# Optimization experiments

Hardware: AMD Instinct MI355X
Metric: run time of the kernel (lower is better)

## Reference

```python
import jax, jax.numpy as jnp
import numpy as np

N_FFTS = (64, 128, 256, 512)
SAMPLE_RATE = 2048
KERNEL_LENGTH = 8
T_SAMPLES = SAMPLE_RATE * KERNEL_LENGTH  # 16384


def _spec_shape(n_fft, n_samples):
    hop = n_fft // 2
    return (n_fft // 2 + 1, n_samples // hop + 1)


_SHAPES = [_spec_shape(n, T_SAMPLES) for n in N_FFTS]
NUM_FREQS = max(s[0] for s in _SHAPES)  # 257
NUM_TIMES = max(s[1] for s in _SHAPES)  # 513


def _spectrogram(x, n_fft):
    """torchaudio.transforms.Spectrogram(n_fft, normalized=True) equivalent.
    Defaults: win_length=n_fft, hop=n_fft//2, hann(periodic), center=True,
    reflect pad, onesided, power=2, normalized='window'.
    x: (..., T) -> (..., n_fft//2+1, n_frames)
    """
    hop = n_fft // 2
    n = jnp.arange(n_fft, dtype=x.dtype)
    w = 0.5 - 0.5 * jnp.cos(2.0 * jnp.pi * n / n_fft)  # periodic hann
    pad = n_fft // 2
    xp = jnp.pad(x, [(0, 0)] * (x.ndim - 1) + [(pad, pad)], mode='reflect')
    n_frames = 1 + (xp.shape[-1] - n_fft) // hop
    idx = hop * jnp.arange(n_frames)[:, None] + jnp.arange(n_fft)[None, :]
    frames = xp[..., idx] * w  # (..., n_frames, n_fft)
    spec = jnp.abs(jnp.fft.rfft(frames, axis=-1)) ** 2 / jnp.sum(w * w)
    return jnp.moveaxis(spec, -1, -2)  # (..., freq, time)


def setup_inputs() -> dict:
    key = jax.random.key(0)
    X = jax.random.normal(key, (64, 2, T_SAMPLES), dtype=jnp.float32)
    return {"X": X}


def reference(X):
    # Remap indices: int(i * shape / max_shape); gather directly from each
    # un-padded spec (indices are always in-range), then elementwise max.
    out = None
    for n_fft, (F_s, N_s) in zip(N_FFTS, _SHAPES):
        spec = _spectrogram(X, n_fft)  # (B, C, F_s, N_s)
        fidx = (jnp.arange(NUM_FREQS) * F_s) // NUM_FREQS  # (M,)
        tidx = (jnp.arange(NUM_TIMES) * N_s) // NUM_TIMES  # (N,)
        remapped = spec[..., fidx[:, None], tidx[None, :]]  # (B, C, M, N)
        out = remapped if out is None else jnp.maximum(out, remapped)
    return out
```

## Files before the change

### kernel.cpp

```cpp
#include <hip/hip_runtime.h>
#include <math.h>

#define T_SAMPLES 16384
#define BC 128
#define NUM_FREQS 257
#define NUM_TIMES 513

#define OFF0 0
#define OFF1 2179584
#define OFF2 4342784
#define OFF3 6522368

typedef float    vf2 __attribute__((ext_vector_type(2)));
typedef float    vf4 __attribute__((ext_vector_type(4)));
typedef vf4 vf4u __attribute__((aligned(4)));
typedef _Float16 vh2 __attribute__((ext_vector_type(2)));
typedef _Float16 vh4 __attribute__((ext_vector_type(4)));

constexpr double CPI = 3.14159265358979323846;
constexpr double ctsin(double x) {
    double x2 = x * x, t = x, s = x;
    for (int n = 1; n <= 12; ++n) { t *= -x2 / (double)((2*n) * (2*n + 1)); s += t; }
    return s;
}
constexpr double ctcos(double x) {
    double x2 = x * x, t = 1.0, s = 1.0;
    for (int n = 1; n <= 12; ++n) { t *= -x2 / (double)((2*n - 1) * (2*n)); s += t; }
    return s;
}
struct Tables {
    float lane_tw[64][10][2];
    float win[4][512];
};
constexpr Tables make_tables() {
    Tables T{};
    for (int l = 0; l < 64; ++l) {
        for (int b = 0; b < 6; ++b) {
            const bool hi = (l >> b) & 1;
            const int  k  = l & ((1 << b) - 1);
            const double a = -2.0 * CPI * (double)k / (double)(1 << (b + 1));
            T.lane_tw[l][b][0] = hi ? (float)ctcos(a) : 1.0f;
            T.lane_tw[l][b][1] = hi ? (float)ctsin(a) : 0.0f;
        }
        for (int i = 0; i < 3; ++i) {
            const double a = -2.0 * CPI * (double)l / (double)(128 << i);
            T.lane_tw[l][6 + i][0] = (float)ctcos(a);
            T.lane_tw[l][6 + i][1] = (float)ctsin(a);
        }
        T.lane_tw[l][9][0] = 0.0f; T.lane_tw[l][9][1] = 0.0f;
    }
    for (int r = 0; r < 4; ++r) {
        const int N = 64 << r;
        for (int n = 0; n < N; ++n) {
            const int m = (2 * n <= N) ? n : n - N;
            const double a = 2.0 * CPI * (double)m / (double)N;
            T.win[r][n] = (float)(0.5 - 0.5 * ctcos(a));
        }
    }
    return T;
}
__device__ __constant__ Tables g_tab = make_tables();

__device__ inline vf2 cmul(vf2 a, vf2 b) {
    vf2 ar = { -a.y, a.x };
    return b.x * a + b.y * ar;
}

template <int CTRL>
__device__ inline float dppf(float x) {
    return __builtin_bit_cast(float,
        __builtin_amdgcn_update_dpp(0, __builtin_bit_cast(int, x),
                                    CTRL, 0xF, 0xF, true));
}

template <int LOGN, int P>
__device__ void fft_tile_body(const float* __restrict__ x, _Float16* __restrict__ spec,
                              int tile, int bc, vf2* __restrict__ zb) {
    constexpr int N     = 1 << LOGN;
    constexpr int HOP   = N / 2;
    constexpr int F     = HOP + 1;
    constexpr int NT    = T_SAMPLES / HOP + 1;
    constexpr int NTP   = (NT + 3) & ~3;
    constexpr int NPAIR = (NT + 1) / 2;
    constexpr int R     = N / 64;
    constexpr int RS2   = N + N / 16 + 1;
    constexpr int KLOOP = P / 4;
    const float NORM4   = 0.25f * 8.0f / (3.0f * (float)N);

    const int tid   = threadIdx.x;
    const int lane  = tid & 63;
    const int wave  = tid >> 6;
    const int pair0 = tile * P;
    const int t0    = pair0 * 2;

    float sgn[6];
    vf2   twe[6];
    vf2   tw6 = {1,0}, tw7 = {1,0}, tw8 = {1,0};
    {
        const vf4* twp = (const vf4*)g_tab.lane_tw[lane];
        vf4 A = twp[0], B = twp[1], C = twp[2], D = twp[3], E = twp[4];
        twe[0] = {A.x, A.y}; twe[1] = {A.z, A.w};
        twe[2] = {B.x, B.y}; twe[3] = {B.z, B.w};
        twe[4] = {C.x, C.y}; twe[5] = {C.z, C.w};
        if constexpr (LOGN >= 7) tw6 = {D.x, D.y};
        if constexpr (LOGN >= 8) tw7 = {D.z, D.w};
        if constexpr (LOGN >= 9) tw8 = {E.x, E.y};
#pragma unroll
        for (int b = 0; b < 6; ++b) sgn[b] = ((lane >> b) & 1) ? -1.0f : 1.0f;
    }

    float wr[R];
#pragma unroll
    for (int r = 0; r < R; ++r) wr[r] = g_tab.win[LOGN - 6][r * 64 + lane];

    const float* xb = x + (size_t)bc * T_SAMPLES;

    vf2  d[KLOOP][R];
    bool act[KLOOP];

#pragma unroll
    for (int q = 0; q < KLOOP; ++q) {
        const int p  = wave * KLOOP + q;
        const int pg = pair0 + p;
        act[q] = (pg < NPAIR);
        if (act[q]) {
            const int t1 = 2 * pg, t2 = t1 + 1;
            const bool refl = (t1 == 0) || (t1 * HOP + N - 1 >= T_SAMPLES) || (t2 >= NT);
            if (!refl) {
                const float* src = xb + t1 * HOP - HOP;
#pragma unroll
                for (int r = 0; r < R; ++r) {
                    int n = r * 64 + lane;
                    vf2 v = { src[n], src[n + HOP] };
                    d[q][r] = v * wr[r];
                }
            } else {
#pragma unroll
                for (int r = 0; r < R; ++r) {
                    int n = r * 64 + lane;
                    int g = t1 * HOP + n - HOP;
                    g = (g < 0) ? -g : g;
                    g = (g >= T_SAMPLES) ? (2 * T_SAMPLES - 2 - g) : g;
                    float re = xb[g] * wr[r];
                    float im = 0.0f;
                    if (t2 < NT) {
                        int h = t2 * HOP + n - HOP;
                        h = (h < 0) ? -h : h;
                        h = (h >= T_SAMPLES) ? (2 * T_SAMPLES - 2 - h) : h;
                        im = xb[h] * wr[r];
                    }
                    d[q][r] = { re, im };
                }
            }
        } else {
#pragma unroll
            for (int r = 0; r < R; ++r) d[q][r] = vf2{0.0f, 0.0f};
        }
    }

    if constexpr (LOGN >= 9) {
        const vf2 u8 = { 0.70710678118654752f, -0.70710678118654752f };
#pragma unroll
        for (int q = 0; q < KLOOP; ++q) {
            vf2 tt = tw8;
#pragma unroll
            for (int r = 0; r < 4; ++r) {
                vf2 a = d[q][r], b = d[q][r + 4];
                d[q][r]     = a + b;
                d[q][r + 4] = cmul(a - b, tt);
                tt = cmul(tt, u8);
            }
        }
    }
    if constexpr (LOGN >= 8) {
        const vf2 t0_ = tw7;
        const vf2 t1_ = { tw7.y, -tw7.x };
#pragma unroll
        for (int q = 0; q < KLOOP; ++q) {
#pragma unroll
            for (int g = 0; g < R; g += 4) {
                { vf2 a = d[q][g],   b = d[q][g+2]; d[q][g]   = a + b; d[q][g+2] = cmul(a - b, t0_); }
                { vf2 a = d[q][g+1], b = d[q][g+3]; d[q][g+1] = a + b; d[q][g+3] = cmul(a - b, t1_); }
            }
        }
    }
    if constexpr (LOGN >= 7) {
#pragma unroll
        for (int q = 0; q < KLOOP; ++q) {
#pragma unroll
            for (int g = 0; g < R; g += 2) {
                vf2 a = d[q][g], b = d[q][g+1];
                d[q][g]   = a + b;
                d[q][g+1] = cmul(a - b, tw6);
            }
        }
    }

#pragma unroll
    for (int b = 5; b >= 2; --b) {
        const int   mask = 1 << b;
        const vf2   w    = twe[b];
        const float s    = sgn[b];
#pragma unroll
        for (int q = 0; q < KLOOP; ++q) {
#pragma unroll
            for (int r = 0; r < R; ++r) {
                vf2 p2;
                p2.x = __shfl_xor(d[q][r].x, mask, 64);
                p2.y = __shfl_xor(d[q][r].y, mask, 64);
                vf2 t  = p2 + d[q][r] * s;
                vf2 tr = { -t.y, t.x };
                d[q][r] = w.x * t + w.y * tr;
            }
        }
    }
    {
        const vf2   w = twe[1];
        const float s = sgn[1];
#pragma unroll
        for (int q = 0; q < KLOOP; ++q) {
#pragma unroll
            for (int r = 0; r < R; ++r) {
                vf2 p2 = { dppf<0x4E>(d[q][r].x), dppf<0x4E>(d[q][r].y) };
                vf2 t  = p2 + d[q][r] * s;
                vf2 tr = { -t.y, t.x };
                d[q][r] = w.x * t + w.y * tr;
            }
        }
    }
    {
        const float s = sgn[0];
#pragma unroll
        for (int q = 0; q < KLOOP; ++q) {
#pragma unroll
            for (int r = 0; r < R; ++r) {
                vf2 p2 = { dppf<0xB1>(d[q][r].x), dppf<0xB1>(d[q][r].y) };
                d[q][r] = p2 + d[q][r] * s;
            }
        }
    }

#pragma unroll
    for (int q = 0; q < KLOOP; ++q) {
        if (act[q]) {
            const int p = wave * KLOOP + q;
#pragma unroll
            for (int r = 0; r < R; ++r) {
                int idx = r * 64 + lane;
                int f   = (int)(__brev((unsigned)idx) >> (32 - LOGN));
                zb[p * RS2 + f + (f >> 4)] = d[q][r];
            }
        }
    }
    __syncthreads();

    _Float16* sbase = spec + (size_t)bc * F * NTP;
    for (int e = tid; e < F * P; e += 256) {
        int f = e / P;
        int p = e & (P - 1);
        int t = t0 + 2 * p;
        if (t < NT) {
            int fn = (N - f) & (N - 1);
            vf2 A = zb[p * RS2 + f  + (f  >> 4)];
            vf2 B = zb[p * RS2 + fn + (fn >> 4)];
            float rx = A.x + B.x, ry = A.y - B.y;
            float sx = A.x - B.x, sy = A.y + B.y;
            vh2 pv = { (_Float16)((rx * rx + ry * ry) * NORM4),
                       (_Float16)((sx * sx + sy * sy) * NORM4) };
            *(vh2*)(sbase + (size_t)f * NTP + t) = pv;
        }
    }
}

__global__ __launch_bounds__(256) void fft_all_kernel(const float* __restrict__ x,
                                                      _Float16* __restrict__ ws) {
    __shared__ vf2 smem[2208];
    const int bx = blockIdx.x;
    const int bc = blockIdx.y;
    if (bx < 9)        fft_tile_body<6, 32>(x, ws + OFF0, bx,      bc, smem);
    else if (bx < 18)  fft_tile_body<7, 16>(x, ws + OFF1, bx - 9,  bc, smem);
    else if (bx < 27)  fft_tile_body<8, 8> (x, ws + OFF2, bx - 18, bc, smem);
    else               fft_tile_body<9, 4> (x, ws + OFF3, bx - 27, bc, smem);
}

__global__ __launch_bounds__(256) void remap_max_kernel(const _Float16* __restrict__ ws,
                                                        float* __restrict__ out) {
    const int JG    = 129;
    const int IG    = 129;
    const int total = BC * IG * JG;
    int idx = blockIdx.x * 256 + threadIdx.x;
    if (idx >= total) return;
    int jg  = idx % JG;
    int rem = idx / JG;
    int ig  = rem % IG;
    int bc  = rem / IG;
    int j0  = jg * 4;
    int i0  = ig * 2;
    const bool fullj = (j0 + 3 < NUM_TIMES);
    const int  ni    = (i0 + 1 < NUM_FREQS) ? 2 : 1;

    float mv[2][4];
#pragma unroll
    for (int ii = 0; ii < 2; ++ii) {
        if (ii < ni) {
            int fi = ((i0 + ii) * 33) / NUM_FREQS;
            const _Float16* p = ws + OFF0 + ((size_t)bc * 33 + fi) * 516 + j0;
            if (fullj) {
                vh4 v = *(const vh4*)p;
                mv[ii][0] = (float)v.x; mv[ii][1] = (float)v.y;
                mv[ii][2] = (float)v.z; mv[ii][3] = (float)v.w;
            } else {
                mv[ii][0] = (float)p[0];
                mv[ii][1] = mv[ii][2] = mv[ii][3] = 0.0f;
            }
        }
    }

    const int fi1a = (i0 * 65) / NUM_FREQS,  fi1b = ((i0 + 1) * 65) / NUM_FREQS;
    const int fi2a = (i0 * 129) / NUM_FREQS, fi2b = ((i0 + 1) * 129) / NUM_FREQS;
    const int fi3a = i0, fi3b = i0 + 1;

#pragma unroll
    for (int k = 0; k < 4; ++k) {
        int j = j0 + k;
        if (j < NUM_TIMES) {
            int ti1 = (j * 257) / NUM_TIMES;
            int ti2 = (j * 129) / NUM_TIMES;
            int ti3 = (j * 65)  / NUM_TIMES;
            const _Float16* b1 = ws + OFF1 + (size_t)bc * 65  * 260 + ti1;
            const _Float16* b2 = ws + OFF2 + (size_t)bc * 129 * 132 + ti2;
            const _Float16* b3 = ws + OFF3 + (size_t)bc * 257 * 68  + ti3;
            mv[0][k] = fmaxf(mv[0][k], (float)b1[(size_t)fi1a * 260]);
            mv[0][k] = fmaxf(mv[0][k], (float)b2[(size_t)fi2a * 132]);
            mv[0][k] = fmaxf(mv[0][k], (float)b3[(size_t)fi3a * 68]);
            if (ni == 2) {
                mv[1][k] = fmaxf(mv[1][k], (float)b1[(size_t)fi1b * 260]);
                mv[1][k] = fmaxf(mv[1][k], (float)b2[(size_t)fi2b * 132]);
                mv[1][k] = fmaxf(mv[1][k], (float)b3[(size_t)fi3b * 68]);
            }
        }
    }

#pragma unroll
    for (int ii = 0; ii < 2; ++ii) {
        if (ii < ni) {
            float* po = out + ((size_t)bc * NUM_FREQS + i0 + ii) * NUM_TIMES + j0;
            if (fullj) {
                vf4 v = { mv[ii][0], mv[ii][1], mv[ii][2], mv[ii][3] };
                *(vf4u*)po = v;
            } else {
                po[0] = mv[ii][0];
            }
        }
    }
}

extern "C" void kernel_launch(void* const* d_in, const int* in_sizes, int n_in,
                              void* d_out, int out_size, void* d_ws, size_t ws_size,
                              hipStream_t stream) {
    const float* x = (const float*)d_in[0];
    _Float16* ws = (_Float16*)d_ws;
    float* out = (float*)d_out;

    fft_all_kernel<<<dim3(36, BC), 256, 0, stream>>>(x, ws);

    const int total = BC * 129 * 129;
    remap_max_kernel<<<(total + 255) / 256, 256, 0, stream>>>(ws, out);
}
```

Measured before the change: 115.3 us.

## Use ds_swizzle for intra-32 FFT butterflies and dedupe remap gather loads

Replaces the xor-shuffle butterfly stages for masks 16, 8 and 4 with ds_swizzle bit-mode patterns, keeping a full-wave shuffle only for mask 32. Swizzle needs no per-lane address computation, unlike a generic shuffle. The remap/max kernel now hoists per-row base pointers and exploits that consecutive output times map to at most two or three distinct source columns, so each thread issues a handful of scalar loads and selects values instead of loading per output element. Row indices are clamped for the edge row so loads stay in bounds without a branch.

```diff
diff --git a/kernel.cpp b/kernel.cpp
--- a/kernel.cpp
+++ b/kernel.cpp
@@ -71,6 +71,42 @@
     return __builtin_bit_cast(float,
         __builtin_amdgcn_update_dpp(0, __builtin_bit_cast(int, x),
                                     CTRL, 0xF, 0xF, true));
+}
+
+template <int PAT>
+__device__ inline float swzf(float x) {
+    return __builtin_bit_cast(float,
+        __builtin_amdgcn_ds_swizzle(__builtin_bit_cast(int, x), PAT));
+}
+
+template <int KL, int RR>
+__device__ inline void stage_shfl32(vf2 (&d)[KL][RR], vf2 w, float s) {
+#pragma unroll
+    for (int q = 0; q < KL; ++q) {
+#pragma unroll
+        for (int r = 0; r < RR; ++r) {
+            vf2 p2;
+            p2.x = __shfl_xor(d[q][r].x, 32, 64);
+            p2.y = __shfl_xor(d[q][r].y, 32, 64);
+            vf2 t  = p2 + d[q][r] * s;
+            vf2 tr = { -t.y, t.x };
+            d[q][r] = w.x * t + w.y * tr;
+        }
+    }
+}
+
+template <int PAT, int KL, int RR>
+__device__ inline void stage_swz(vf2 (&d)[KL][RR], vf2 w, float s) {
+#pragma unroll
+    for (int q = 0; q < KL; ++q) {
+#pragma unroll
+        for (int r = 0; r < RR; ++r) {
+            vf2 p2 = { swzf<PAT>(d[q][r].x), swzf<PAT>(d[q][r].y) };
+            vf2 t  = p2 + d[q][r] * s;
+            vf2 tr = { -t.y, t.x };
+            d[q][r] = w.x * t + w.y * tr;
+        }
+    }
 }
 
 template <int LOGN, int P>
@@ -196,24 +232,10 @@
         }
     }
 
-#pragma unroll
-    for (int b = 5; b >= 2; --b) {
-        const int   mask = 1 << b;
-        const vf2   w    = twe[b];
-        const float s    = sgn[b];
-#pragma unroll
-        for (int q = 0; q < KLOOP; ++q) {
-#pragma unroll
-            for (int r = 0; r < R; ++r) {
-                vf2 p2;
-                p2.x = __shfl_xor(d[q][r].x, mask, 64);
-                p2.y = __shfl_xor(d[q][r].y, mask, 64);
-                vf2 t  = p2 + d[q][r] * s;
-                vf2 tr = { -t.y, t.x };
-                d[q][r] = w.x * t + w.y * tr;
-            }
-        }
-    }
+    stage_shfl32(d, twe[5], sgn[5]);
+    stage_swz<0x401F>(d, twe[4], sgn[4]);
+    stage_swz<0x201F>(d, twe[3], sgn[3]);
+    stage_swz<0x101F>(d, twe[2], sgn[2]);
     {
         const vf2   w = twe[1];
         const float s = sgn[1];
@@ -302,6 +324,7 @@
     float mv[2][4];
 #pragma unroll
     for (int ii = 0; ii < 2; ++ii) {
+        mv[ii][0] = mv[ii][1] = mv[ii][2] = mv[ii][3] = 0.0f;
         if (ii < ni) {
             int fi = ((i0 + ii) * 33) / NUM_FREQS;
             const _Float16* p = ws + OFF0 + ((size_t)bc * 33 + fi) * 516 + j0;
@@ -311,33 +334,55 @@
                 mv[ii][2] = (float)v.z; mv[ii][3] = (float)v.w;
             } else {
                 mv[ii][0] = (float)p[0];
-                mv[ii][1] = mv[ii][2] = mv[ii][3] = 0.0f;
-            }
-        }
-    }
-
-    const int fi1a = (i0 * 65) / NUM_FREQS,  fi1b = ((i0 + 1) * 65) / NUM_FREQS;
-    const int fi2a = (i0 * 129) / NUM_FREQS, fi2b = ((i0 + 1) * 129) / NUM_FREQS;
-    const int fi3a = i0, fi3b = i0 + 1;
+            }
+        }
+    }
+
+    const int fi1a = (i0 * 65) / NUM_FREQS;
+    const int fi2a = (i0 * 129) / NUM_FREQS;
+    const int fi3a = i0;
+    int fi1b = ((i0 + 1) * 65) / NUM_FREQS;  if (fi1b > 64)  fi1b = 64;
+    int fi2b = ((i0 + 1) * 129) / NUM_FREQS; if (fi2b > 128) fi2b = 128;
+    int fi3b = i0 + 1;                       if (fi3b > 256) fi3b = 256;
+
+    const _Float16* p1a = ws + OFF1 + ((size_t)bc * 65  + fi1a) * 260;
+    const _Float16* p1b = ws + OFF1 + ((size_t)bc * 65  + fi1b) * 260;
+    const _Float16* p2a = ws + OFF2 + ((size_t)bc * 129 + fi2a) * 132;
+    const _Float16* p2b = ws + OFF2 + ((size_t)bc * 129 + fi2b) * 132;
+    const _Float16* p3a = ws + OFF3 + ((size_t)bc * 257 + fi3a) * 68;
+    const _Float16* p3b = ws + OFF3 + ((size_t)bc * 257 + fi3b) * 68;
+
+    int t1[4], t2[4], t3[4];
+#pragma unroll
+    for (int k = 0; k < 4; ++k) {
+        int j = j0 + k;
+        t1[k] = (j * 257) / NUM_TIMES;
+        t2[k] = (j * 129) / NUM_TIMES;
+        t3[k] = (j * 65)  / NUM_TIMES;
+    }
+    float a1A = (float)p1a[t1[0]], m1A = (float)p1a[t1[0] + 1], b1A = (float)p1a[t1[3]];
+    float a2A = (float)p2a[t2[0]], b2A = (float)p2a[t2[3]];
+    float a3A = (float)p3a[t3[0]], b3A = (float)p3a[t3[3]];
+    float a1B = (float)p1b[t1[0]], m1B = (float)p1b[t1[0] + 1], b1B = (float)p1b[t1[3]];
+    float a2B = (float)p2b[t2[0]], b2B = (float)p2b[t2[3]];
+    float a3B = (float)p3b[t3[0]], b3B = (float)p3b[t3[3]];
 
 #pragma unroll
     for (int k = 0; k < 4; ++k) {
         int j = j0 + k;
         if (j < NUM_TIMES) {
-            int ti1 = (j * 257) / NUM_TIMES;
-            int ti2 = (j * 129) / NUM_TIMES;
-            int ti3 = (j * 65)  / NUM_TIMES;
-            const _Float16* b1 = ws + OFF1 + (size_t)bc * 65  * 260 + ti1;
-            const _Float16* b2 = ws + OFF2 + (size_t)bc * 129 * 132 + ti2;
-            const _Float16* b3 = ws + OFF3 + (size_t)bc * 257 * 68  + ti3;
-            mv[0][k] = fmaxf(mv[0][k], (float)b1[(size_t)fi1a * 260]);
-            mv[0][k] = fmaxf(mv[0][k], (float)b2[(size_t)fi2a * 132]);
-            mv[0][k] = fmaxf(mv[0][k], (float)b3[(size_t)fi3a * 68]);
-            if (ni == 2) {
-                mv[1][k] = fmaxf(mv[1][k], (float)b1[(size_t)fi1b * 260]);
-                mv[1][k] = fmaxf(mv[1][k], (float)b2[(size_t)fi2b * 132]);
-                mv[1][k] = fmaxf(mv[1][k], (float)b3[(size_t)fi3b * 68]);
-            }
+            float v1A = (t1[k] == t1[0]) ? a1A : ((t1[k] == t1[3]) ? b1A : m1A);
+            float v2A = (t2[k] == t2[0]) ? a2A : b2A;
+            float v3A = (t3[k] == t3[0]) ? a3A : b3A;
+            mv[0][k] = fmaxf(mv[0][k], v1A);
+            mv[0][k] = fmaxf(mv[0][k], v2A);
+            mv[0][k] = fmaxf(mv[0][k], v3A);
+            float v1B = (t1[k] == t1[0]) ? a1B : ((t1[k] == t1[3]) ? b1B : m1B);
+            float v2B = (t2[k] == t2[0]) ? a2B : b2B;
+            float v3B = (t3[k] == t3[0]) ? a3B : b3B;
+            mv[1][k] = fmaxf(mv[1][k], v1B);
+            mv[1][k] = fmaxf(mv[1][k], v2B);
+            mv[1][k] = fmaxf(mv[1][k], v3B);
         }
     }
 
```

Result: faster. 109.7 us (median of 2 runs) (-4.9%).
